# Kernel tuning notes

Hardware: AMD Instinct MI355X
Metric: run time of the kernel (lower is better)

The kernel has to match this reference:

```python
import jax, jax.numpy as jnp
import numpy as np

N = 8192
IN_F = 512
OUT_F = 128
ALPHA = 0.2  # leaky relu negative slope
NEG_BIG = -1e10
RND_SCALE = 1e5


def setup_inputs() -> dict:
    key = jax.random.key(0)
    k1, k2, k3, k4, k5 = jax.random.split(key, 5)
    h = jax.random.normal(k1, (N, IN_F), dtype=jnp.float32)
    adj = jax.random.randint(k2, (N, N), 0, 2, dtype=jnp.int32)
    W = jax.random.normal(k3, (IN_F, OUT_F), dtype=jnp.float32) * 0.05
    a = jax.random.normal(k4, (2 * OUT_F, 1), dtype=jnp.float32) * 0.1
    # rnd in original is 1e5*(rand-0.5); same distribution here
    rnd = RND_SCALE * (jax.random.uniform(k5, (N, OUT_F), dtype=jnp.float32) - 0.5)
    return {"h": h, "adj": adj, "W": W, "a": a, "rnd": rnd}


def reference(h, adj, W, a, rnd):
    Wh = h @ W                              # [N, OUT_F]
    Wh1 = Wh @ a[:OUT_F, :]                 # [N, 1]
    Wh2 = Wh @ a[OUT_F:, :]                 # [N, 1]
    e = jax.nn.leaky_relu(Wh1 + Wh2.T, negative_slope=ALPHA)  # [N, N]
    attention = jnp.where(adj > 0, e, NEG_BIG)
    attention = jax.nn.softmax(attention, axis=1)
    h_prime = attention @ Wh                # [N, OUT_F]
    h_prime = (h_prime + rnd) / RND_SCALE
    return jax.nn.elu(h_prime)
```

## Files before the change

kernel.cpp:

```cpp
#include <hip/hip_runtime.h>

#define N 8192
#define IN_F 512
#define OUT_F 128
#define SPLITK 16
#define LOG2E 1.4426950408889634f
#define LN2 0.6931471805599453f

typedef __attribute__((ext_vector_type(4))) float f32x4;
typedef __attribute__((ext_vector_type(8))) short bf16x8;
typedef __attribute__((ext_vector_type(8))) unsigned short u16x8;

__device__ __forceinline__ short f2bf(float f) {
    union { float f; unsigned u; } c; c.f = f;
    unsigned r = c.u + 0x7FFFu + ((c.u >> 16) & 1u);
    return (short)(r >> 16);
}

__device__ __forceinline__ float exp2fast(float x) {
#if __has_builtin(__builtin_amdgcn_exp2f)
    return __builtin_amdgcn_exp2f(x);
#else
    return __expf(x * LN2);
#endif
}

__device__ __forceinline__ void load_lds16(const void* g, void* l) {
    __builtin_amdgcn_global_load_lds((const __attribute__((address_space(1))) unsigned*)g,
                                     (__attribute__((address_space(3))) unsigned*)l,
                                     16, 0, 0);
}

__global__ __launch_bounds__(256) void conv_W(const float* __restrict__ W, short* __restrict__ WT) {
    int idx = blockIdx.x * 256 + threadIdx.x;
    int n = idx & (OUT_F - 1);
    int k = idx >> 7;
    WT[(size_t)n * IN_F + k] = f2bf(W[idx]);
}

__global__ __launch_bounds__(256) void gemm_hW(const float* __restrict__ h,
                                               const short* __restrict__ WT,
                                               const float* __restrict__ a,
                                               short* __restrict__ WhT,
                                               float* __restrict__ sOut,
                                               float* __restrict__ tOut) {
    const int tid = threadIdx.x;
    const int wave = tid >> 6, lane = tid & 63;
    const int row16 = lane & 15, kgrp = lane >> 4;
    const int m0 = blockIdx.x * 16;
    const int kbase = wave * 128;

    f32x4 acc[8] = {};
    const float4* hp = (const float4*)(h + (size_t)(m0 + row16) * IN_F + kbase);

#pragma unroll
    for (int kk = 0; kk < 128; kk += 32) {
        float4 u0 = hp[kk / 4 + kgrp * 2];
        float4 u1 = hp[kk / 4 + kgrp * 2 + 1];
        bf16x8 af;
        af[0] = f2bf(u0.x); af[1] = f2bf(u0.y); af[2] = f2bf(u0.z); af[3] = f2bf(u0.w);
        af[4] = f2bf(u1.x); af[5] = f2bf(u1.y); af[6] = f2bf(u1.z); af[7] = f2bf(u1.w);
#pragma unroll
        for (int nt = 0; nt < 8; nt++) {
            bf16x8 bf_ = *(const bf16x8*)(WT + (size_t)(nt * 16 + row16) * IN_F + kbase + kk + kgrp * 8);
            acc[nt] = __builtin_amdgcn_mfma_f32_16x16x32_bf16(af, bf_, acc[nt], 0, 0, 0);
        }
    }

    __shared__ float red[4][16][132];
#pragma unroll
    for (int nt = 0; nt < 8; nt++)
#pragma unroll
        for (int r = 0; r < 4; r++)
            red[wave][kgrp * 4 + r][nt * 16 + row16] = acc[nt][r];
    __syncthreads();

    const int row = tid >> 4, seg = tid & 15;
    float v[8];
#pragma unroll
    for (int e = 0; e < 8; e++) {
        int c = seg * 8 + e;
        v[e] = red[0][row][c] + red[1][row][c] + red[2][row][c] + red[3][row][c];
    }
    float sp = 0.f, tp = 0.f;
#pragma unroll
    for (int e = 0; e < 8; e++) {
        sp += v[e] * a[seg * 8 + e];
        tp += v[e] * a[OUT_F + seg * 8 + e];
    }
    sp += __shfl_xor(sp, 1); tp += __shfl_xor(tp, 1);
    sp += __shfl_xor(sp, 2); tp += __shfl_xor(tp, 2);
    sp += __shfl_xor(sp, 4); tp += __shfl_xor(tp, 4);
    sp += __shfl_xor(sp, 8); tp += __shfl_xor(tp, 8);
    if (seg == 0) {
        sOut[m0 + row] = sp * LOG2E;
        tOut[m0 + row] = tp * LOG2E;
    }
#pragma unroll
    for (int e = 0; e < 8; e++)
        WhT[(size_t)(seg * 8 + e) * N + m0 + row] = f2bf(v[e]);
}

__global__ __launch_bounds__(256, 3) void attn(const int* __restrict__ adj,
                                               const short* __restrict__ WhT,
                                               const float* __restrict__ s,
                                               const float* __restrict__ t,
                                               unsigned short* __restrict__ num,
                                               float* __restrict__ lpart) {
    const int tid = threadIdx.x;
    const int wave = tid >> 6, lane = tid & 63;
    const int row16 = lane & 15, kgrp = lane >> 4;
    const int m0 = blockIdx.x * 128 + wave * 32;
    const int ks = blockIdx.y * 512;

    __shared__ short Bs[2][2][128 * 32];
    __shared__ float tl[512];

    tl[tid] = t[ks + tid];
    if (tid < 256) tl[tid + 256] = t[ks + tid + 256];

    float s_m[2];
    const int4* ap4[2];
#pragma unroll
    for (int mi = 0; mi < 2; mi++) {
        int m = m0 + mi * 16 + row16;
        s_m[mi] = s[m];
        ap4[mi] = (const int4*)(adj + (size_t)m * N + ks);
    }

    auto stageB = [&](int sup, int par) {
        const int k0 = ks + sup * 64;
#pragma unroll
        for (int d = 0; d < 2; d++)
#pragma unroll
            for (int q = 0; q < 2; q++) {
                int nrow = wave * 32 + q * 16 + (lane >> 2);
                const short* g = WhT + (size_t)nrow * N + k0 + d * 32 + (lane & 3) * 8;
                load_lds16(g, &Bs[par][d][(wave * 32 + q * 16) * 32]);
            }
    };

    f32x4 acc[2][8] = {};
    float lsum[2] = {0.f, 0.f};

    int4 nx[2][2];
#pragma unroll
    for (int mi = 0; mi < 2; mi++)
#pragma unroll
        for (int q = 0; q < 2; q++) nx[mi][q] = ap4[mi][kgrp * 2 + q];
    stageB(0, 0);
    __syncthreads();

    for (int sp = 0; sp < 8; sp++) {
        const int par = sp & 1;
#pragma unroll
        for (int d = 0; d < 2; d++) {
            const int g = sp * 2 + d;
            int4 cu[2][2];
#pragma unroll
            for (int mi = 0; mi < 2; mi++)
#pragma unroll
                for (int q = 0; q < 2; q++) cu[mi][q] = nx[mi][q];
            if (g + 1 < 16) {
#pragma unroll
                for (int mi = 0; mi < 2; mi++)
#pragma unroll
                    for (int q = 0; q < 2; q++)
                        nx[mi][q] = ap4[mi][(g + 1) * 8 + kgrp * 2 + q];
            }
            if (d == 0 && sp + 1 < 8) stageB(sp + 1, par ^ 1);

            const float* tp = tl + g * 32 + kgrp * 8;
            float4 tA = *(const float4*)tp;
            float4 tB = *(const float4*)(tp + 4);
            float tv[8] = { tA.x, tA.y, tA.z, tA.w, tB.x, tB.y, tB.z, tB.w };

            bf16x8 bfr[8];
            const short* base = &Bs[par][d][0];
#pragma unroll
            for (int ni = 0; ni < 8; ni++)
                bfr[ni] = *(const bf16x8*)(base + (ni * 16 + row16) * 32 + kgrp * 8);

#pragma unroll
            for (int mi = 0; mi < 2; mi++) {
                const int* ai = (const int*)cu[mi];
                unsigned pu[8];
#pragma unroll
                for (int e = 0; e < 8; e++) {
                    float x = s_m[mi] + tv[e];
                    x = fmaxf(x, 0.2f * x);
                    float p = exp2fast(x);
                    unsigned u = __float_as_uint(p) & 0xFFFF0000u;
                    u = ai[e] > 0 ? u : 0u;
                    lsum[mi] += __uint_as_float(u);
                    pu[e] = u;
                }
                bf16x8 af;
                unsigned* au = (unsigned*)&af;
#pragma unroll
                for (int q = 0; q < 4; q++) au[q] = (pu[2 * q] >> 16) | pu[2 * q + 1];
#pragma unroll
                for (int ni = 0; ni < 8; ni++)
                    acc[mi][ni] = __builtin_amdgcn_mfma_f32_16x16x32_bf16(af, bfr[ni], acc[mi][ni], 0, 0, 0);
            }
        }
        __syncthreads();
    }

#pragma unroll
    for (int mi = 0; mi < 2; mi++) {
        float v = lsum[mi];
        v += __shfl_xor(v, 16);
        v += __shfl_xor(v, 32);
        if (kgrp == 0) lpart[(size_t)blockIdx.y * N + m0 + mi * 16 + row16] = v;
    }

    unsigned short* np_ = num + (size_t)blockIdx.y * N * OUT_F;
#pragma unroll
    for (int mi = 0; mi < 2; mi++) {
        int mb = m0 + mi * 16 + kgrp * 4;
#pragma unroll
        for (int ni = 0; ni < 8; ni++) {
            int n = ni * 16 + row16;
#pragma unroll
            for (int r = 0; r < 4; r++)
                np_[(size_t)(mb + r) * OUT_F + n] = (unsigned short)f2bf(acc[mi][ni][r]);
        }
    }
}

__global__ __launch_bounds__(256) void finalize(const unsigned short* __restrict__ num,
                                                const float* __restrict__ lpart,
                                                const float* __restrict__ rnd,
                                                float* __restrict__ out) {
    int idx = blockIdx.x * 256 + threadIdx.x;
    int m = idx >> 4;
    int c = (idx & 15) * 8;
    size_t g = (size_t)m * OUT_F + c;

    float nm[8] = {};
#pragma unroll
    for (int bk = 0; bk < SPLITK; bk++) {
        u16x8 v = *(const u16x8*)(num + (size_t)bk * N * OUT_F + g);
#pragma unroll
        for (int e = 0; e < 8; e++) nm[e] += __uint_as_float((unsigned)v[e] << 16);
    }
    float l = 0.f;
#pragma unroll
    for (int bk = 0; bk < SPLITK; bk++) l += lpart[(size_t)bk * N + m];
    float inv = 1.f / fmaxf(l, 1e-30f);

    float4 r0 = *(const float4*)(rnd + g);
    float4 r1 = *(const float4*)(rnd + g + 4);
    float rv[8] = { r0.x, r0.y, r0.z, r0.w, r1.x, r1.y, r1.z, r1.w };
    float ov[8];
#pragma unroll
    for (int e = 0; e < 8; e++) {
        float x = (nm[e] * inv + rv[e]) * 1e-5f;
        ov[e] = x > 0.f ? x : __expf(x) - 1.f;
    }
    *(float4*)(out + g)     = make_float4(ov[0], ov[1], ov[2], ov[3]);
    *(float4*)(out + g + 4) = make_float4(ov[4], ov[5], ov[6], ov[7]);
}

extern "C" void kernel_launch(void* const* d_in, const int* in_sizes, int n_in,
                              void* d_out, int out_size, void* d_ws, size_t ws_size,
                              hipStream_t stream) {
    const float* h   = (const float*)d_in[0];
    const int*   adj = (const int*)d_in[1];
    const float* W   = (const float*)d_in[2];
    const float* a   = (const float*)d_in[3];
    const float* rnd = (const float*)d_in[4];
    float* out = (float*)d_out;

    char* w = (char*)d_ws;
    short* WT    = (short*)(w);
    short* WhT   = (short*)(w + 131072);
    float* sv    = (float*)(w + 2228224);
    float* tv    = (float*)(w + 2260992);
    float* lpart = (float*)(w + 2293760);
    unsigned short* num = (unsigned short*)(w + 2818048);

    conv_W  <<<256, 256, 0, stream>>>(W, WT);
    gemm_hW <<<512, 256, 0, stream>>>(h, WT, a, WhT, sv, tv);
    attn    <<<dim3(64, SPLITK), 256, 0, stream>>>(adj, WhT, sv, tv, num, lpart);
    finalize<<<(N * OUT_F / 8) / 256, 256, 0, stream>>>(num, lpart, rnd, out);
}
```

Baseline: 441.4 us.

## Pack adjacency into bitmask in prepass and retile attention kernel

Adds a kernel that reads the int32 adjacency matrix once and packs it into a bitmask, one byte per 8 columns. The attention kernel then reads this compact mask instead of the int adjacency. The attention kernel also changes shape: 16 rows per wave instead of 32, split-K drops from 16 to 8 with 1024-column chunks, occupancy hint goes from 3 to 4, and there is one barrier per staged sub-block. Full adjacency traffic still happens once in the prepass, but the attention phase moves far less data and partial-sum traffic halves. In exchange, each WhT tile is now reused across fewer rows.

```diff
diff --git a/kernel.cpp b/kernel.cpp
--- a/kernel.cpp
+++ b/kernel.cpp
@@ -3,7 +3,9 @@
 #define N 8192
 #define IN_F 512
 #define OUT_F 128
-#define SPLITK 16
+#define NW (N / 8)
+#define SPLITK 8
+#define KC 1024
 #define LOG2E 1.4426950408889634f
 #define LN2 0.6931471805599453f
 
@@ -36,6 +38,24 @@
     int n = idx & (OUT_F - 1);
     int k = idx >> 7;
     WT[(size_t)n * IN_F + k] = f2bf(W[idx]);
+}
+
+__global__ __launch_bounds__(256) void mkmask(const int* __restrict__ adj,
+                                              unsigned char* __restrict__ maskR) {
+    const int wave = threadIdx.x >> 6, lane = threadIdx.x & 63;
+    const size_t m = (size_t)blockIdx.x * 4 + wave;
+    const int4* ap = (const int4*)(adj + m * N);
+    unsigned char* mp = maskR + m * NW;
+#pragma unroll 4
+    for (int it = 0; it < 16; it++) {
+        int b4 = it * 128 + lane * 2;
+        int4 a0 = ap[b4], a1 = ap[b4 + 1];
+        unsigned b = (unsigned)(a0.x > 0) | ((unsigned)(a0.y > 0) << 1) |
+                     ((unsigned)(a0.z > 0) << 2) | ((unsigned)(a0.w > 0) << 3) |
+                     ((unsigned)(a1.x > 0) << 4) | ((unsigned)(a1.y > 0) << 5) |
+                     ((unsigned)(a1.z > 0) << 6) | ((unsigned)(a1.w > 0) << 7);
+        mp[it * 64 + lane] = (unsigned char)b;
+    }
 }
 
 __global__ __launch_bounds__(256) void gemm_hW(const float* __restrict__ h,
@@ -101,7 +121,7 @@
         WhT[(size_t)(seg * 8 + e) * N + m0 + row] = f2bf(v[e]);
 }
 
-__global__ __launch_bounds__(256, 3) void attn(const int* __restrict__ adj,
+__global__ __launch_bounds__(256, 4) void attn(const unsigned char* __restrict__ maskR,
                                                const short* __restrict__ WhT,
                                                const float* __restrict__ s,
                                                const float* __restrict__ t,
@@ -110,23 +130,18 @@
     const int tid = threadIdx.x;
     const int wave = tid >> 6, lane = tid & 63;
     const int row16 = lane & 15, kgrp = lane >> 4;
-    const int m0 = blockIdx.x * 128 + wave * 32;
-    const int ks = blockIdx.y * 512;
+    const int m0 = blockIdx.x * 64 + wave * 16;
+    const int m  = m0 + row16;
+    const int ks = blockIdx.y * KC;
 
     __shared__ short Bs[2][2][128 * 32];
-    __shared__ float tl[512];
-
-    tl[tid] = t[ks + tid];
-    if (tid < 256) tl[tid + 256] = t[ks + tid + 256];
-
-    float s_m[2];
-    const int4* ap4[2];
-#pragma unroll
-    for (int mi = 0; mi < 2; mi++) {
-        int m = m0 + mi * 16 + row16;
-        s_m[mi] = s[m];
-        ap4[mi] = (const int4*)(adj + (size_t)m * N + ks);
-    }
+    __shared__ float tl[KC];
+
+    for (int i = tid; i < KC; i += 256) tl[i] = t[ks + i];
+
+    const float s_m = s[m];
+    const int4* mp = (const int4*)(maskR + (size_t)m * NW + (ks >> 3));
+    int4 mcur = mp[0], mnxt = mp[1];
 
     auto stageB = [&](int sup, int par) {
         const int k0 = ks + sup * 64;
@@ -140,59 +155,44 @@
             }
     };
 
-    f32x4 acc[2][8] = {};
-    float lsum[2] = {0.f, 0.f};
-
-    int4 nx[2][2];
-#pragma unroll
-    for (int mi = 0; mi < 2; mi++)
-#pragma unroll
-        for (int q = 0; q < 2; q++) nx[mi][q] = ap4[mi][kgrp * 2 + q];
+    f32x4 acc[8] = {};
+    float lsum = 0.f;
+
     stageB(0, 0);
     __syncthreads();
 
-    for (int sp = 0; sp < 8; sp++) {
-        const int par = sp & 1;
-#pragma unroll
-        for (int d = 0; d < 2; d++) {
-            const int g = sp * 2 + d;
-            int4 cu[2][2];
-#pragma unroll
-            for (int mi = 0; mi < 2; mi++)
-#pragma unroll
-                for (int q = 0; q < 2; q++) cu[mi][q] = nx[mi][q];
-            if (g + 1 < 16) {
-#pragma unroll
-                for (int mi = 0; mi < 2; mi++)
-#pragma unroll
-                    for (int q = 0; q < 2; q++)
-                        nx[mi][q] = ap4[mi][(g + 1) * 8 + kgrp * 2 + q];
-            }
-            if (d == 0 && sp + 1 < 8) stageB(sp + 1, par ^ 1);
-
-            const float* tp = tl + g * 32 + kgrp * 8;
-            float4 tA = *(const float4*)tp;
-            float4 tB = *(const float4*)(tp + 4);
-            float tv[8] = { tA.x, tA.y, tA.z, tA.w, tB.x, tB.y, tB.z, tB.w };
-
-            bf16x8 bfr[8];
-            const short* base = &Bs[par][d][0];
-#pragma unroll
-            for (int ni = 0; ni < 8; ni++)
-                bfr[ni] = *(const bf16x8*)(base + (ni * 16 + row16) * 32 + kgrp * 8);
-
-#pragma unroll
-            for (int mi = 0; mi < 2; mi++) {
-                const int* ai = (const int*)cu[mi];
+    for (int sp2 = 0; sp2 < 8; sp2++) {
+#pragma unroll
+        for (int ss = 0; ss < 2; ss++) {
+            const int sp = sp2 * 2 + ss;
+            const int par = sp & 1;
+            if (sp + 1 < 16) stageB(sp + 1, par ^ 1);
+#pragma unroll
+            for (int d = 0; d < 2; d++) {
+                const int g = sp * 2 + d;
+                const unsigned dw = (unsigned)((const int*)&mcur)[ss * 2 + d];
+                const unsigned mbyte = (dw >> (kgrp * 8)) & 0xFFu;
+
+                const float* tp = tl + g * 32 + kgrp * 8;
+                float4 tA = *(const float4*)tp;
+                float4 tB = *(const float4*)(tp + 4);
+                float tv[8] = { tA.x, tA.y, tA.z, tA.w, tB.x, tB.y, tB.z, tB.w };
+
+                bf16x8 bfr[8];
+                const short* base = &Bs[par][d][0];
+#pragma unroll
+                for (int ni = 0; ni < 8; ni++)
+                    bfr[ni] = *(const bf16x8*)(base + (ni * 16 + row16) * 32 + kgrp * 8);
+
                 unsigned pu[8];
 #pragma unroll
                 for (int e = 0; e < 8; e++) {
-                    float x = s_m[mi] + tv[e];
+                    float x = s_m + tv[e];
                     x = fmaxf(x, 0.2f * x);
                     float p = exp2fast(x);
                     unsigned u = __float_as_uint(p) & 0xFFFF0000u;
-                    u = ai[e] > 0 ? u : 0u;
-                    lsum[mi] += __uint_as_float(u);
+                    u = ((mbyte >> e) & 1u) ? u : 0u;
+                    lsum += __uint_as_float(u);
                     pu[e] = u;
                 }
                 bf16x8 af;
@@ -201,31 +201,28 @@
                 for (int q = 0; q < 4; q++) au[q] = (pu[2 * q] >> 16) | pu[2 * q + 1];
 #pragma unroll
                 for (int ni = 0; ni < 8; ni++)
-                    acc[mi][ni] = __builtin_amdgcn_mfma_f32_16x16x32_bf16(af, bfr[ni], acc[mi][ni], 0, 0, 0);
+                    acc[ni] = __builtin_amdgcn_mfma_f32_16x16x32_bf16(af, bfr[ni], acc[ni], 0, 0, 0);
             }
+            __syncthreads();
         }
-        __syncthreads();
-    }
-
-#pragma unroll
-    for (int mi = 0; mi < 2; mi++) {
-        float v = lsum[mi];
+        mcur = mnxt;
+        if (sp2 + 2 < 8) mnxt = mp[sp2 + 2];
+    }
+
+    {
+        float v = lsum;
         v += __shfl_xor(v, 16);
         v += __shfl_xor(v, 32);
-        if (kgrp == 0) lpart[(size_t)blockIdx.y * N + m0 + mi * 16 + row16] = v;
-    }
-
-    unsigned short* np_ = num + (size_t)blockIdx.y * N * OUT_F;
-#pragma unroll
-    for (int mi = 0; mi < 2; mi++) {
-        int mb = m0 + mi * 16 + kgrp * 4;
-#pragma unroll
-        for (int ni = 0; ni < 8; ni++) {
-            int n = ni * 16 + row16;
-#pragma unroll
-            for (int r = 0; r < 4; r++)
-                np_[(size_t)(mb + r) * OUT_F + n] = (unsigned short)f2bf(acc[mi][ni][r]);
-        }
+        if (kgrp == 0) lpart[(size_t)blockIdx.y * N + m] = v;
+    }
+
+    unsigned short* np_ = num + ((size_t)blockIdx.y * N + m0) * OUT_F;
+#pragma unroll
+    for (int ni = 0; ni < 8; ni++) {
+        int n = ni * 16 + row16;
+#pragma unroll
+        for (int r = 0; r < 4; r++)
+            np_[(size_t)(kgrp * 4 + r) * OUT_F + n] = (unsigned short)f2bf(acc[ni][r]);
     }
 }
 
@@ -279,10 +276,12 @@
     float* sv    = (float*)(w + 2228224);
     float* tv    = (float*)(w + 2260992);
     float* lpart = (float*)(w + 2293760);
-    unsigned short* num = (unsigned short*)(w + 2818048);
+    unsigned char* maskR = (unsigned char*)(w + 2555904);
+    unsigned short* num  = (unsigned short*)(w + 10944512);
 
     conv_W  <<<256, 256, 0, stream>>>(W, WT);
+    mkmask  <<<2048, 256, 0, stream>>>(adj, maskR);
     gemm_hW <<<512, 256, 0, stream>>>(h, WT, a, WhT, sv, tv);
-    attn    <<<dim3(64, SPLITK), 256, 0, stream>>>(adj, WhT, sv, tv, num, lpart);
+    attn    <<<dim3(128, SPLITK), 256, 0, stream>>>(maskR, WhT, sv, tv, num, lpart);
     finalize<<<(N * OUT_F / 8) / 256, 256, 0, stream>>>(num, lpart, rnd, out);
 }
```

Result: faster. 427.3 us (-3.2%).
